# Kernel tuning notes

Measured on AMD Instinct MI355X. Metric: run time of the kernel, lower is better.

## Reference

```python
import jax, jax.numpy as jnp
import numpy as np

B, D, E, NF, FD, H = 8192, 1024, 6, 32, 32, 256
MINK, MAXK = 1, 4

def _lin(a, w, b):
    return a @ w.T + b

def setup_inputs():
    key = jax.random.key(0)
    it = iter(jax.random.split(key, 60))
    def nrm(shape, s=0.02):
        return jax.random.normal(next(it), shape, jnp.float32) * s
    z = lambda *s: jnp.zeros(s, jnp.float32)
    return dict(
        x=jax.random.normal(next(it), (B, D), jnp.float32),
        esp_patterns=nrm((E, D), 1.0),
        sim_w1=nrm((D // 2, D)), sim_b1=z(D // 2),
        sim_w2=nrm((E, D // 2)), sim_b2=z(E),
        rout_w1=nrm((D // 2, D + E)), rout_b1=z(D // 2),
        rout_w2=nrm((E, D // 2)), rout_b2=z(E),
        kpred_w1=nrm((16, 6)), kpred_b1=z(16),
        kpred_w2=nrm((1, 16)), kpred_b2=z(1),
        sp_v_w=nrm((D, D)), sp_v_b=z(D),
        sp_o_w=nrm((D, D)), sp_o_b=z(D),
        sp_q1_w=nrm((D, D)), sp_q1_b=z(D),
        sp_q2_w=nrm((D, D)), sp_q2_b=z(D),
        de_w1=nrm((H, D)), de_b1=z(H),
        de_w2=nrm((D, H)), de_b2=z(D),
        de_g_w=nrm((D, D)), de_g_b=z(D),
        cf_in_w=nrm((3 * FD, FD)), cf_in_b=z(3 * FD),
        cf_o_w=nrm((FD, FD)), cf_o_b=z(FD),
        cf_f_w=nrm((FD, FD)), cf_f_b=z(FD),
        hf_w1=nrm((H, D)), hf_b1=z(H),
        hf_w2=nrm((D, H)), hf_b2=z(D),
        tc_w=nrm((4, 1, 3), 0.2), tc_b=z(4),
        tf_w=nrm((1, 4), 0.2), tf_b=z(1),
        lt_w1=nrm((H, D)), lt_b1=z(H),
        lt_w2=nrm((D, H)), lt_b2=z(D),
        op_w=nrm((D, D)), op_b=z(D),
    )

def reference(x, esp_patterns, sim_w1, sim_b1, sim_w2, sim_b2, rout_w1, rout_b1, rout_w2, rout_b2,
              kpred_w1, kpred_b1, kpred_w2, kpred_b2, sp_v_w, sp_v_b, sp_o_w, sp_o_b,
              sp_q1_w, sp_q1_b, sp_q2_w, sp_q2_b, de_w1, de_b1, de_w2, de_b2, de_g_w, de_g_b,
              cf_in_w, cf_in_b, cf_o_w, cf_o_b, cf_f_w, cf_f_b, hf_w1, hf_b1, hf_w2, hf_b2,
              tc_w, tc_b, tf_w, tf_b, lt_w1, lt_b1, lt_w2, lt_b2, op_w, op_b):
    # ---- FeatureAnalyzer ----
    sparsity = (x == 0).astype(jnp.float32).mean(-1)
    var_u = jnp.var(x, axis=-1, ddof=1)            # torch default unbiased var
    magnitude = jnp.abs(x).max(-1)
    norm = jnp.linalg.norm(x, axis=-1)
    mean = x.mean(-1, keepdims=True)
    std = jnp.sqrt(var_u[:, None] + 1e-8)
    skew = (((x - mean) / std) ** 3).mean(-1)
    s_abs = -jnp.sort(-jnp.abs(x), axis=-1)        # descending
    top20 = int(0.2 * D)
    conc = s_abs[:, :top20].sum(-1) / (s_abs.sum(-1) + 1e-8)
    feats = jnp.stack([sparsity, var_u, magnitude, norm, skew, conc], -1)  # (B,6)
    # ---- IntelligentRouter ----
    spec = jax.nn.sigmoid(x @ esp_patterns.T + _lin(jax.nn.relu(_lin(x, sim_w1, sim_b1)), sim_w2, sim_b2))
    probs = jax.nn.softmax(_lin(jax.nn.relu(_lin(jnp.concatenate([x, spec], -1), rout_w1, rout_b1)), rout_w2, rout_b2), -1)
    k_ratio = jax.nn.sigmoid(_lin(jax.nn.relu(_lin(feats, kpred_w1, kpred_b1)), kpred_w2, kpred_b2))[:, 0]
    k_vals = MINK + (MAXK - MINK) * k_ratio
    k = jnp.clip(jnp.floor(jnp.median(k_vals)), MINK, MAXK).astype(jnp.int32)  # int(median) truncation
    tp, ti = jax.lax.top_k(probs, MAXK)
    gmask = jnp.arange(MAXK) < k
    gates = jax.nn.softmax(jnp.where(gmask, tp, -jnp.inf), -1)  # (B,MAXK)
    # ---- experts (eval mode: dropout = identity) ----
    # SparseQuadraticExpert: seq-len-1 MHA collapses to V->out projections
    att = _lin(_lin(x, sp_v_w, sp_v_b), sp_o_w, sp_o_b)
    e_sp = _lin(jax.nn.relu(_lin(att * x, sp_q1_w, sp_q1_b)), sp_q2_w, sp_q2_b)
    # DenseQuadraticExpert
    e_de = _lin(jax.nn.relu(_lin(x, de_w1, de_b1)), de_w2, de_b2) + jax.nn.sigmoid(_lin(x, de_g_w, de_g_b)) * x
    # CrossFieldQuadraticExpert: single-head attention over fields
    xf = x.reshape(-1, NF, FD)
    q, kk, v = jnp.split(_lin(xf, cf_in_w, cf_in_b), 3, axis=-1)
    attn = jax.nn.softmax(jnp.einsum('bqd,bkd->bqk', q, kk) / jnp.sqrt(jnp.float32(FD)), -1)
    att_f = _lin(jnp.einsum('bqk,bkd->bqd', attn, v), cf_o_w, cf_o_b)
    e_cf = _lin(att_f * xf, cf_f_w, cf_f_b).reshape(-1, D)
    # HighFreqQuadraticExpert
    filt = _lin(jnp.tanh(_lin(x, hf_w1, hf_b1)), hf_w2, hf_b2)
    e_hf = x + (filt - x) * x
    # TemporalQuadraticExpert (AdaptiveAvgPool1d(D) on length-D input == identity)
    conv = jax.nn.relu(jax.lax.conv_general_dilated(x[:, None, :], tc_w, (1,), [(1, 1)], dimension_numbers=('NCH', 'OIH', 'NCH')) + tc_b[None, :, None])
    wts = jax.nn.sigmoid(_lin(conv.transpose(0, 2, 1), tf_w, tf_b))[..., 0]  # (B,D)
    e_tp = (x * wts) * x
    # LongTailQuadraticExpert
    t = _lin(jax.nn.elu(_lin(x, lt_w1, lt_b1)), lt_w2, lt_b2)
    e_lt = jnp.sign(x) * jnp.sqrt(jnp.abs(t * x) + 1e-8)
    # ---- dispatch + combine ----
    stack = jnp.stack([e_sp, e_de, e_cf, e_hf, e_tp, e_lt], axis=1)  # (B,E,D)
    sel = jnp.take_along_axis(stack, ti[:, :, None], axis=1)         # (B,MAXK,D)
    comb = (gates[:, :, None] * sel).sum(1)
    return _lin(comb, op_w, op_b) + x  # output projection + residual; Identity norm (batch_norm=False)
```

## Files before the change

kernel.cpp:

```cpp
#include <hip/hip_runtime.h>
#include <stdint.h>

typedef unsigned short u16;
typedef __attribute__((ext_vector_type(2))) float f32x2;
typedef __attribute__((ext_vector_type(4))) float f32x4;
typedef __attribute__((ext_vector_type(4))) unsigned short u16x4;
typedef __attribute__((ext_vector_type(8))) short short8;

#define DEV static __device__ __forceinline__

DEV float bf2f(u16 u){ union{unsigned int i; float f;} v; v.i=((unsigned int)u)<<16; return v.f; }
DEV u16 f2bf(float f){ union{float f; unsigned int i;} v; v.f=f; unsigned int u=v.i;
  return (u16)((u + 0x7FFFu + ((u>>16)&1u))>>16); }
DEV float wred(float v){ for(int o=32;o;o>>=1) v += __shfl_xor(v,o); return v; }
DEV float wredmax(float v){ for(int o=32;o;o>>=1) v = fmaxf(v,__shfl_xor(v,o)); return v; }
DEV int wredi(int v){ for(int o=32;o;o>>=1) v += __shfl_xor(v,o); return v; }

DEV void gload16(const void* g, void* l){
  __builtin_amdgcn_global_load_lds((const __attribute__((address_space(1))) unsigned int*)g,
                                   (__attribute__((address_space(3))) unsigned int*)l, 16, 0, 0);
}

DEV float actf(int ACT, float v){
  if(ACT==1) return v>0.f?v:0.f;
  if(ACT==2) return 1.f/(1.f+__expf(-v));
  if(ACT==3) return tanhf(v);
  if(ACT==4) return v>0.f?v:(__expf(v)-1.f);
  return v;
}

__global__ void cvt_kernel(const float* __restrict__ s, u16* __restrict__ d, int n4){
  for(int i=blockIdx.x*blockDim.x+threadIdx.x; i<n4; i+=gridDim.x*blockDim.x){
    f32x4 v=((const f32x4*)s)[i];
    u16x4 o;
    #pragma unroll
    for(int j=0;j<4;++j) o[j]=f2bf(v[j]);
    ((u16x4*)d)[i]=o;
  }
}

__global__ void cvt6_kernel(
    const float* __restrict__ s0, const float* __restrict__ s1, const float* __restrict__ s2,
    const float* __restrict__ s3, const float* __restrict__ s4, const float* __restrict__ s5,
    u16* __restrict__ d0, u16* __restrict__ d1, u16* __restrict__ d2,
    u16* __restrict__ d3, u16* __restrict__ d4, u16* __restrict__ d5, int n4each){
  const float* ss[6]={s0,s1,s2,s3,s4,s5};
  u16* dd[6]={d0,d1,d2,d3,d4,d5};
  const int total=6*n4each;
  for(int i=blockIdx.x*blockDim.x+threadIdx.x; i<total; i+=gridDim.x*blockDim.x){
    int b=i/n4each, r=i-b*n4each;
    f32x4 v=((const f32x4*)ss[b])[r];
    u16x4 o;
    #pragma unroll
    for(int j=0;j<4;++j) o[j]=f2bf(v[j]);
    ((u16x4*)dd[b])[r]=o;
  }
}

__global__ void cvt_split(const float* __restrict__ s, u16* __restrict__ hi, u16* __restrict__ lo, int n4){
  for(int i=blockIdx.x*blockDim.x+threadIdx.x; i<n4; i+=gridDim.x*blockDim.x){
    f32x4 v=((const f32x4*)s)[i];
    u16x4 h,l;
    #pragma unroll
    for(int j=0;j<4;++j){ h[j]=f2bf(v[j]); l[j]=f2bf(v[j]-bf2f(h[j])); }
    ((u16x4*)hi)[i]=h; ((u16x4*)lo)[i]=l;
  }
}

__global__ void cvt_split_rw1(const float* __restrict__ src, u16* __restrict__ hi, u16* __restrict__ lo){
  for(int i=blockIdx.x*blockDim.x+threadIdx.x; i<512*1024; i+=gridDim.x*blockDim.x){
    int r=i>>10, c=i&1023;
    float v=src[(size_t)r*1030+c];
    u16 h=f2bf(v);
    hi[i]=h; lo[i]=f2bf(v-bf2f(h));
  }
}

__global__ __launch_bounds__(256) void transpose_bf(const float* __restrict__ src, u16* __restrict__ dst){
  __shared__ float t[32][33];
  const int bx=blockIdx.x&31, by=blockIdx.x>>5;
  const int lx=threadIdx.x&31, ly=threadIdx.x>>5;
  #pragma unroll
  for(int r=0;r<4;++r)
    t[ly+8*r][lx] = src[(size_t)(by*32+ly+8*r)*1024 + bx*32+lx];
  __syncthreads();
  #pragma unroll
  for(int r=0;r<4;++r)
    dst[(size_t)(bx*32+ly+8*r)*1024 + by*32+lx] = f2bf(t[lx][ly+8*r]);
}

__global__ __launch_bounds__(256) void bias_comp(const float* __restrict__ ow, const float* __restrict__ vb,
    const float* __restrict__ ob, float* __restrict__ bc){
  const int wv=threadIdx.x>>6, lane=threadIdx.x&63;
  const int rowi=blockIdx.x*4+wv;
  float s=0.f;
  const float* wr=ow+(size_t)rowi*1024;
  #pragma unroll
  for(int j=0;j<16;++j) s+=wr[j*64+lane]*vb[j*64+lane];
  s=wred(s);
  if(lane==0) bc[rowi]=ob[rowi]+s;
}

__global__ void pack_b768(const float* __restrict__ b0, const float* __restrict__ b1,
                          const float* __restrict__ b2, float* __restrict__ o){
  int i=blockIdx.x*blockDim.x+threadIdx.x;
  if(i<256) o[i]=b0[i];
  else if(i<512) o[i]=b1[i-256];
  else if(i<768) o[i]=b2[i-512];
}

__global__ void pack_b1024(const float* __restrict__ b0, const float* __restrict__ b1, float* __restrict__ o){
  int i=blockIdx.x*blockDim.x+threadIdx.x;
  if(i<512) o[i]=b0[i];
  else if(i<1024) o[i]=b1[i-512];
}

template<int ACT, int EPI>
__global__ __launch_bounds__(256) void gemm_bt(
    const u16* __restrict__ A, const u16* __restrict__ W,
    const float* __restrict__ bias, const u16* __restrict__ auxb,
    const float* __restrict__ auxf, const float* __restrict__ wsel,
    float* __restrict__ comb, void* __restrict__ Cv, int M, int N, int K, int lda)
{
  __shared__ __align__(16) u16 lA[128*64];
  __shared__ __align__(16) u16 lB[128*64];
  const int tid=threadIdx.x, lane=tid&63, wv=tid>>6;
  const int wr=wv>>1, wc=wv&1;
  const int bn=blockIdx.x*128, bm=blockIdx.y*128;
  f32x4 acc[4][4];
  #pragma unroll
  for(int m=0;m<4;++m){
    #pragma unroll
    for(int n=0;n<4;++n) acc[m][n]=(f32x4)0.f;
  }
  const int srow = wv*8 + (lane>>3);
  const int scol = (lane&7)*8;
  for(int kt=0;kt<K;kt+=64){
    #pragma unroll
    for(int i=0;i<4;++i){
      gload16(A + (size_t)(bm + i*32 + srow)*lda + kt + scol, &lA[(i*32 + wv*8)*64]);
      gload16(W + (size_t)(bn + i*32 + srow)*K + kt + scol, &lB[(i*32 + wv*8)*64]);
    }
    __syncthreads();
    #pragma unroll
    for(int kk=0;kk<2;++kk){
      const int fr=lane&15, kc=kk*32+(lane>>4)*8;
      short8 af[4], bfr[4];
      #pragma unroll
      for(int m=0;m<4;++m) af[m]=*(const short8*)&lA[(wr*64+m*16+fr)*64+kc];
      #pragma unroll
      for(int n=0;n<4;++n) bfr[n]=*(const short8*)&lB[(wc*64+n*16+fr)*64+kc];
      #pragma unroll
      for(int m=0;m<4;++m){
        #pragma unroll
        for(int n=0;n<4;++n)
          acc[m][n]=__builtin_amdgcn_mfma_f32_16x16x32_bf16(af[m],bfr[n],acc[m][n],0,0,0);
      }
    }
    __syncthreads();
  }
  const int fr=lane&15, fq=lane>>4;
  #pragma unroll
  for(int m=0;m<4;++m){
    #pragma unroll
    for(int n=0;n<4;++n){
      const int col = bn + wc*64 + n*16 + fr;
      const float bv = bias ? bias[col] : 0.f;
      #pragma unroll
      for(int j=0;j<4;++j){
        const int row = bm + wr*64 + m*16 + fq*4 + j;
        const size_t idx = (size_t)row*N+col;
        float v = acc[m][n][j] + bv;
        if(ACT==5){
          v = (col<256) ? fmaxf(v,0.f) : (col<512 ? tanhf(v) : (v>0.f?v:(__expf(v)-1.f)));
        } else v = actf(ACT, v);
        if(EPI==0){ ((u16*)Cv)[idx]=f2bf(v); }
        else if(EPI==1){ ((float*)Cv)[idx]=v; }
        else if(EPI==2){ ((u16*)Cv)[idx]=f2bf(v*auxf[idx]); }
        else if(EPI==3){ comb[idx]=wsel[row*6+0]*v; }
        else if(EPI==4){ comb[idx]+=wsel[row*6+1]*(v + bf2f(auxb[idx])*auxf[idx]); }
        else if(EPI==5){ float x0=auxf[idx]; comb[idx]+=wsel[row*6+3]*(x0+(v-x0)*x0); }
        else if(EPI==6){
          float x0=auxf[idx];
          float sg=(x0>0.f)?1.f:((x0<0.f)?-1.f:0.f);
          comb[idx]+=wsel[row*6+5]*sg*sqrtf(fabsf(v*x0)+1e-8f);
        }
        else { ((float*)Cv)[idx]=v+auxf[idx]; }
      }
    }
  }
}

__global__ __launch_bounds__(256) void gemm_split2(
    const u16* __restrict__ Ah, const u16* __restrict__ Al,
    const u16* __restrict__ Wh, const u16* __restrict__ Wl,
    const float* __restrict__ bias, float* __restrict__ C, int M, int N, int K)
{
  const int LDL=40;
  __shared__ __align__(16) u16 lAh[128*40], lAl[128*40], lBh[128*40], lBl[128*40];
  const int tid=threadIdx.x, lane=tid&63, wv=tid>>6;
  const int wr=wv>>1, wc=wv&1;
  const int nwg=gridDim.x;
  const int wg=(blockIdx.x%8)*(nwg/8)+blockIdx.x/8;
  const int bx=wg&7, by=wg>>3;
  const int bn=bx*128, bm=by*128;
  f32x4 acc[4][4];
  #pragma unroll
  for(int m=0;m<4;++m){
    #pragma unroll
    for(int n=0;n<4;++n) acc[m][n]=(f32x4)0.f;
  }
  const int srow=tid>>2, scol=(tid&3)*8;
  for(int kt=0;kt<K;kt+=32){
    short8 rah[2],ral[2],rbh[2],rbl[2];
    #pragma unroll
    for(int i=0;i<2;++i){
      size_t ao=(size_t)(bm+i*64+srow)*K+kt+scol;
      size_t bo=(size_t)(bn+i*64+srow)*K+kt+scol;
      rah[i]=*(const short8*)(Ah+ao); ral[i]=*(const short8*)(Al+ao);
      rbh[i]=*(const short8*)(Wh+bo); rbl[i]=*(const short8*)(Wl+bo);
    }
    __syncthreads();
    #pragma unroll
    for(int i=0;i<2;++i){
      int d=(i*64+srow)*LDL+scol;
      *(short8*)&lAh[d]=rah[i]; *(short8*)&lAl[d]=ral[i];
      *(short8*)&lBh[d]=rbh[i]; *(short8*)&lBl[d]=rbl[i];
    }
    __syncthreads();
    const int fr=lane&15, kc=(lane>>4)*8;
    short8 ah[4],al[4],bh[4],bl[4];
    #pragma unroll
    for(int m=0;m<4;++m){ int r=(wr*64+m*16+fr)*LDL+kc; ah[m]=*(const short8*)&lAh[r]; al[m]=*(const short8*)&lAl[r]; }
    #pragma unroll
    for(int n=0;n<4;++n){ int r=(wc*64+n*16+fr)*LDL+kc; bh[n]=*(const short8*)&lBh[r]; bl[n]=*(const short8*)&lBl[r]; }
    #pragma unroll
    for(int m=0;m<4;++m){
      #pragma unroll
      for(int n=0;n<4;++n){
        acc[m][n]=__builtin_amdgcn_mfma_f32_16x16x32_bf16(ah[m],bh[n],acc[m][n],0,0,0);
        acc[m][n]=__builtin_amdgcn_mfma_f32_16x16x32_bf16(ah[m],bl[n],acc[m][n],0,0,0);
        acc[m][n]=__builtin_amdgcn_mfma_f32_16x16x32_bf16(al[m],bh[n],acc[m][n],0,0,0);
      }
    }
  }
  const int fr=lane&15, fq=lane>>4;
  #pragma unroll
  for(int m=0;m<4;++m){
    #pragma unroll
    for(int n=0;n<4;++n){
      const int col = bn + wc*64 + n*16 + fr;
      const float bv = bias[col];
      #pragma unroll
      for(int j=0;j<4;++j){
        const int row = bm + wr*64 + m*16 + fq*4 + j;
        float v = acc[m][n][j] + bv;
        if(col<512) v=fmaxf(v,0.f);
        C[(size_t)row*N+col] = v;
      }
    }
  }
}

__global__ __launch_bounds__(256) void feats_kernel(const float* __restrict__ x,
    const float* __restrict__ kw1, const float* __restrict__ kb1,
    const float* __restrict__ kw2, const float* __restrict__ kb2,
    float* __restrict__ kvals)
{
  const int lane=threadIdx.x&63, wv=threadIdx.x>>6;
  const int row=blockIdx.x*4+wv;
  const float* xr=x+(size_t)row*1024;
  float xv[16]; unsigned int cd[16];
  float s=0.f, ss=0.f, sa=0.f, nz=0.f, amax=0.f;
  #pragma unroll
  for(int t=0;t<4;++t){
    f32x4 v=((const f32x4*)xr)[t*64+lane];
    #pragma unroll
    for(int j=0;j<4;++j){
      float f=v[j];
      union{float f;unsigned int i;} c; c.f=f;
      xv[t*4+j]=f; cd[t*4+j]=c.i&0x7fffffffu;
      s+=f; ss+=f*f; float a=fabsf(f); sa+=a; amax=fmaxf(amax,a); if(f==0.f) nz+=1.f;
    }
  }
  s=wred(s); ss=wred(ss); sa=wred(sa); nz=wred(nz); amax=wredmax(amax);
  const float mean=s/1024.f;
  const float var=(ss - s*mean)/1023.f;
  const float inv=1.f/sqrtf(var+1e-8f);
  float sk=0.f;
  #pragma unroll
  for(int j=0;j<16;++j){ float z=(xv[j]-mean)*inv; sk+=z*z*z; }
  sk=wred(sk);
  unsigned int lo=0u, hi=0x7f800000u;
  while(hi-lo>1u){
    unsigned int mid=(lo+hi)>>1;
    int c=0;
    #pragma unroll
    for(int j=0;j<16;++j) c += (cd[j] >= mid);
    c=wredi(c);
    if(c>=204) lo=mid; else hi=mid;
  }
  const unsigned int T=lo;
  float sg=0.f, cg=0.f;
  #pragma unroll
  for(int j=0;j<16;++j){ if(cd[j] > T){ sg+=fabsf(xv[j]); cg+=1.f; } }
  sg=wred(sg); cg=wred(cg);
  if(lane==0){
    union{unsigned int i;float f;} tv; tv.i=T;
    float conc=(sg + (204.f-cg)*tv.f)/(sa + 1e-8f);
    float feats[6]={ nz/1024.f, var, amax, sqrtf(ss), sk/1024.f, conc };
    float out=kb2[0];
    #pragma unroll
    for(int i=0;i<16;++i){
      float hv=kb1[i];
      #pragma unroll
      for(int j=0;j<6;++j) hv+=kw1[i*6+j]*feats[j];
      hv=fmaxf(hv,0.f);
      out+=kw2[i]*hv;
    }
    kvals[row]=1.f + 3.f*(1.f/(1.f+__expf(-out)));
  }
}

__global__ __launch_bounds__(256) void median_kernel(const float* __restrict__ kvals, int* __restrict__ kint){
  __shared__ unsigned int v[8192];
  __shared__ int hist4[4*257];
  __shared__ unsigned int selT;
  __shared__ int selR;
  const int tid=threadIdx.x, lane=tid&63, wv=tid>>6;
  for(int i=tid;i<8192;i+=256){ union{float f;unsigned int u;} c; c.f=kvals[i]; v[i]=c.u; }
  __syncthreads();
  unsigned int res[2];
  for(int t=0;t<2;++t){
    int r = 8192 - (4096+t) + 1;
    unsigned int prefix=0u;
    for(int lvl=0;lvl<4;++lvl){
      const int shift=24-lvl*8;
      const unsigned int pmask = (lvl==0)?0u:(0xFFFFFFFFu<<(shift+8));
      for(int i=tid;i<4*257;i+=256) hist4[i]=0;
      __syncthreads();
      for(int i=tid;i<8192;i+=256){
        unsigned int c=v[i];
        if((c&pmask)==prefix) atomicAdd(&hist4[wv*257+((c>>shift)&0xFFu)],1);
      }
      __syncthreads();
      if(wv==0){
        int h[4]; int ls=0;
        #pragma unroll
        for(int b=0;b<4;++b){
          int bin=lane*4+b;
          h[b]=hist4[bin]+hist4[257+bin]+hist4[514+bin]+hist4[771+bin];
          ls+=h[b];
        }
        int pfx=ls;
        #pragma unroll
        for(int off=1;off<64;off<<=1){ int tt=__shfl_up(pfx,off); if(lane>=off) pfx+=tt; }
        int total=__shfl(pfx,63);
        int cgt = total - pfx;
        #pragma unroll
        for(int b=3;b>=0;--b){
          if(cgt < r && r <= cgt + h[b]){
            selT = prefix | ((unsigned int)(lane*4+b)<<shift);
            selR = r - cgt;
          }
          cgt += h[b];
        }
      }
      __syncthreads();
      prefix=selT; r=selR;
      __syncthreads();
    }
    res[t]=prefix;
  }
  if(tid==0){
    union{unsigned int u; float f;} a,b; a.u=res[0]; b.u=res[1];
    float med=0.5f*(a.f+b.f);
    int k=(int)floorf(med);
    k = k<1?1:(k>4?4:k);
    *kint=k;
  }
}

__global__ __launch_bounds__(256) void spec_kernel(const float* __restrict__ x, const float* __restrict__ h,
    const float* __restrict__ esp, const float* __restrict__ w2, const float* __restrict__ b2,
    float* __restrict__ spec){
  const int wv=threadIdx.x>>6, lane=threadIdx.x&63;
  const int row=blockIdx.x*4+wv;
  const float* xr=x+(size_t)row*1024;
  const float* hr=h+(size_t)row*1024;
  float xv[16], hv[8];
  #pragma unroll
  for(int j=0;j<16;++j) xv[j]=xr[j*64+lane];
  #pragma unroll
  for(int j=0;j<8;++j) hv[j]=hr[j*64+lane];
  for(int e=0;e<6;++e){
    float s=0.f;
    #pragma unroll
    for(int j=0;j<16;++j) s+=xv[j]*esp[e*1024+j*64+lane];
    #pragma unroll
    for(int j=0;j<8;++j) s+=hv[j]*w2[e*512+j*64+lane];
    s=wred(s);
    if(lane==0) spec[row*6+e]=1.f/(1.f+__expf(-(s+b2[e])));
  }
}

__global__ void rout_fix(float* __restrict__ h, const float* __restrict__ spec, const float* __restrict__ rw1){
  const int total=8192*128;
  for(int i=blockIdx.x*blockDim.x+threadIdx.x;i<total;i+=gridDim.x*blockDim.x){
    int row=i>>7, j0=(i&127)*4;
    const float* sp=&spec[row*6];
    f32x4 hv=*(f32x4*)&h[(size_t)row*1024+512+j0];
    #pragma unroll
    for(int j=0;j<4;++j){
      float v=hv[j];
      int col=j0+j;
      #pragma unroll
      for(int e=0;e<6;++e) v+=sp[e]*rw1[(size_t)col*1030+1024+e];
      hv[j]=fmaxf(v,0.f);
    }
    *(f32x4*)&h[(size_t)row*1024+512+j0]=hv;
  }
}

__global__ __launch_bounds__(256) void probs_kernel(const float* __restrict__ h, const float* __restrict__ w2,
    const float* __restrict__ b2, float* __restrict__ probs){
  const int wv=threadIdx.x>>6, lane=threadIdx.x&63;
  const int row=blockIdx.x*4+wv;
  const float* hr=h+(size_t)row*1024+512;
  float hv[8];
  #pragma unroll
  for(int j=0;j<8;++j) hv[j]=hr[j*64+lane];
  float lg[6];
  #pragma unroll
  for(int e=0;e<6;++e){
    float s=0.f;
    #pragma unroll
    for(int j=0;j<8;++j) s+=hv[j]*w2[e*512+j*64+lane];
    lg[e]=wred(s)+b2[e];
  }
  if(lane==0){
    float m=lg[0];
    #pragma unroll
    for(int e=1;e<6;++e) m=fmaxf(m,lg[e]);
    float den=0.f, ex[6];
    #pragma unroll
    for(int e=0;e<6;++e){ ex[e]=__expf(lg[e]-m); den+=ex[e]; }
    #pragma unroll
    for(int e=0;e<6;++e) probs[row*6+e]=ex[e]/den;
  }
}

__global__ void gates_kernel(const float* __restrict__ probs, const int* __restrict__ kint,
                             float* __restrict__ wsel){
  const int r=blockIdx.x*blockDim.x+threadIdx.x;
  if(r>=8192) return;
  const int k=*kint;
  float p[6];
  #pragma unroll
  for(int e=0;e<6;++e) p[e]=probs[r*6+e];
  float w[6]={0,0,0,0,0,0};
  bool used[6]={false,false,false,false,false,false};
  int idx[4]; float val[4];
  #pragma unroll
  for(int j=0;j<4;++j){
    int bi=0; float bv=-1e30f;
    #pragma unroll
    for(int e=0;e<6;++e) if(!used[e] && p[e]>bv){ bv=p[e]; bi=e; }
    used[bi]=true; idx[j]=bi; val[j]=bv;
  }
  float m=val[0], den=0.f, g[4]={0,0,0,0};
  for(int j=0;j<k;++j){ g[j]=__expf(val[j]-m); den+=g[j]; }
  for(int j=0;j<k;++j) w[idx[j]]=g[j]/den;
  #pragma unroll
  for(int e=0;e<6;++e) wsel[r*6+e]=w[e];
}

__global__ __launch_bounds__(256) void cf_kernel(const float* __restrict__ x,
    const float* __restrict__ w_in, const float* __restrict__ b_in,
    const float* __restrict__ w_o, const float* __restrict__ b_o,
    const float* __restrict__ w_f, const float* __restrict__ b_f,
    const float* __restrict__ wsel, float* __restrict__ comb){
  __shared__ __align__(16) u16 smem[6400 + 4*6144];
  const int tid=threadIdx.x, wv=tid>>6, lane=tid&63;
  const int fr=lane&15, fq=lane>>4;
  for(int i=tid;i<5120;i+=256){
    float v=(i<3072)? w_in[i] : (i<4096? w_o[i-3072] : w_f[i-4096]);
    smem[(i>>5)*40 + (i&31)] = f2bf(v);
  }
  u16* wb   = smem + 6400 + wv*6144;
  float* xfl= (float*)wb;
  u16* bufA = wb + 2304;
  u16* bufB = bufA + 1280;
  u16* bufC = bufB + 1280;
  const int row = blockIdx.x*4 + wv;
  const float* xr = x + (size_t)row*1024;
  #pragma unroll
  for(int t=0;t<4;++t){
    f32x4 v = ((const f32x4*)xr)[t*64+lane];
    int e=(t*64+lane)*4;
    *(f32x4*)&xfl[(e>>5)*36 + (e&31)] = v;
  }
  __syncthreads();
  short8 xa[2];
  #pragma unroll
  for(int ft=0;ft<2;++ft){
    f32x4 a=*(const f32x4*)&xfl[(ft*16+fr)*36 + fq*8];
    f32x4 b=*(const f32x4*)&xfl[(ft*16+fr)*36 + fq*8 + 4];
    short8 s;
    s[0]=(short)f2bf(a[0]); s[1]=(short)f2bf(a[1]); s[2]=(short)f2bf(a[2]); s[3]=(short)f2bf(a[3]);
    s[4]=(short)f2bf(b[0]); s[5]=(short)f2bf(b[1]); s[6]=(short)f2bf(b[2]); s[7]=(short)f2bf(b[3]);
    xa[ft]=s;
  }
  f32x4 acc1[2][6];
  #pragma unroll
  for(int ct=0;ct<6;++ct){
    short8 wfrag=*(const short8*)&smem[(ct*16+fr)*40 + fq*8];
    #pragma unroll
    for(int ft=0;ft<2;++ft)
      acc1[ft][ct]=__builtin_amdgcn_mfma_f32_16x16x32_bf16(xa[ft],wfrag,(f32x4)0.f,0,0,0);
  }
  float bi[6];
  #pragma unroll
  for(int ct=0;ct<6;++ct) bi[ct]=b_in[ct*16+fr];
  #pragma unroll
  for(int ct=0;ct<6;++ct){
    #pragma unroll
    for(int ft=0;ft<2;++ft){
      #pragma unroll
      for(int j=0;j<4;++j){
        u16 h=f2bf(acc1[ft][ct][j]+bi[ct]);
        int rg=ft*16+fq*4+j, cg=ct*16+fr;
        if(cg<32)      bufA[rg*40+cg]=h;
        else if(cg<64) bufB[rg*40+(cg-32)]=h;
        else           bufC[(cg-64)*40+rg]=h;
      }
    }
  }
  __syncthreads();
  short8 qa0=*(const short8*)&bufA[fr*40+fq*8];
  short8 qa1=*(const short8*)&bufA[(16+fr)*40+fq*8];
  short8 kb0=*(const short8*)&bufB[fr*40+fq*8];
  short8 kb1=*(const short8*)&bufB[(16+fr)*40+fq*8];
  f32x4 aS[2][2];
  aS[0][0]=__builtin_amdgcn_mfma_f32_16x16x32_bf16(qa0,kb0,(f32x4)0.f,0,0,0);
  aS[0][1]=__builtin_amdgcn_mfma_f32_16x16x32_bf16(qa0,kb1,(f32x4)0.f,0,0,0);
  aS[1][0]=__builtin_amdgcn_mfma_f32_16x16x32_bf16(qa1,kb0,(f32x4)0.f,0,0,0);
  aS[1][1]=__builtin_amdgcn_mfma_f32_16x16x32_bf16(qa1,kb1,(f32x4)0.f,0,0,0);
  const float scale=0.17677669529663687f;
  #pragma unroll
  for(int rt=0;rt<2;++rt){
    #pragma unroll
    for(int j=0;j<4;++j){
      float e0=aS[rt][0][j]*scale, e1=aS[rt][1][j]*scale;
      float m=fmaxf(e0,e1);
      #pragma unroll
      for(int o=1;o<16;o<<=1) m=fmaxf(m,__shfl_xor(m,o));
      e0=__expf(e0-m); e1=__expf(e1-m);
      float den=e0+e1;
      #pragma unroll
      for(int o=1;o<16;o<<=1) den+=__shfl_xor(den,o);
      float inv=1.f/den;
      bufA[(rt*16+fq*4+j)*40 + fr]      = f2bf(e0*inv);
      bufA[(rt*16+fq*4+j)*40 + 16+fr]   = f2bf(e1*inv);
    }
  }
  __syncthreads();
  short8 pa0=*(const short8*)&bufA[fr*40+fq*8];
  short8 pa1=*(const short8*)&bufA[(16+fr)*40+fq*8];
  short8 vb0=*(const short8*)&bufC[fr*40+fq*8];
  short8 vb1=*(const short8*)&bufC[(16+fr)*40+fq*8];
  f32x4 aA[2][2];
  aA[0][0]=__builtin_amdgcn_mfma_f32_16x16x32_bf16(pa0,vb0,(f32x4)0.f,0,0,0);
  aA[0][1]=__builtin_amdgcn_mfma_f32_16x16x32_bf16(pa0,vb1,(f32x4)0.f,0,0,0);
  aA[1][0]=__builtin_amdgcn_mfma_f32_16x16x32_bf16(pa1,vb0,(f32x4)0.f,0,0,0);
  aA[1][1]=__builtin_amdgcn_mfma_f32_16x16x32_bf16(pa1,vb1,(f32x4)0.f,0,0,0);
  #pragma unroll
  for(int rt=0;rt<2;++rt)
    #pragma unroll
    for(int dt=0;dt<2;++dt)
      #pragma unroll
      for(int j=0;j<4;++j)
        bufB[(rt*16+fq*4+j)*40 + dt*16+fr]=f2bf(aA[rt][dt][j]);
  __syncthreads();
  short8 aa0=*(const short8*)&bufB[fr*40+fq*8];
  short8 aa1=*(const short8*)&bufB[(16+fr)*40+fq*8];
  short8 ob0=*(const short8*)&smem[(96+fr)*40+fq*8];
  short8 ob1=*(const short8*)&smem[(112+fr)*40+fq*8];
  f32x4 aF[2][2];
  aF[0][0]=__builtin_amdgcn_mfma_f32_16x16x32_bf16(aa0,ob0,(f32x4)0.f,0,0,0);
  aF[0][1]=__builtin_amdgcn_mfma_f32_16x16x32_bf16(aa0,ob1,(f32x4)0.f,0,0,0);
  aF[1][0]=__builtin_amdgcn_mfma_f32_16x16x32_bf16(aa1,ob0,(f32x4)0.f,0,0,0);
  aF[1][1]=__builtin_amdgcn_mfma_f32_16x16x32_bf16(aa1,ob1,(f32x4)0.f,0,0,0);
  float bo[2]={b_o[fr], b_o[16+fr]};
  #pragma unroll
  for(int rt=0;rt<2;++rt){
    #pragma unroll
    for(int dt=0;dt<2;++dt){
      #pragma unroll
      for(int j=0;j<4;++j){
        int fld=rt*16+fq*4+j, d=dt*16+fr;
        float attf=aF[rt][dt][j]+bo[dt];
        bufC[fld*40+d]=f2bf(attf*xfl[fld*36+d]);
      }
    }
  }
  __syncthreads();
  short8 pr0=*(const short8*)&bufC[fr*40+fq*8];
  short8 pr1=*(const short8*)&bufC[(16+fr)*40+fq*8];
  short8 fb0=*(const short8*)&smem[(128+fr)*40+fq*8];
  short8 fb1=*(const short8*)&smem[(144+fr)*40+fq*8];
  f32x4 aE[2][2];
  aE[0][0]=__builtin_amdgcn_mfma_f32_16x16x32_bf16(pr0,fb0,(f32x4)0.f,0,0,0);
  aE[0][1]=__builtin_amdgcn_mfma_f32_16x16x32_bf16(pr0,fb1,(f32x4)0.f,0,0,0);
  aE[1][0]=__builtin_amdgcn_mfma_f32_16x16x32_bf16(pr1,fb0,(f32x4)0.f,0,0,0);
  aE[1][1]=__builtin_amdgcn_mfma_f32_16x16x32_bf16(pr1,fb1,(f32x4)0.f,0,0,0);
  float bff[2]={b_f[fr], b_f[16+fr]};
  const float w2=wsel[row*6+2];
  float* cb=&comb[(size_t)row*1024];
  #pragma unroll
  for(int rt=0;rt<2;++rt){
    #pragma unroll
    for(int dt=0;dt<2;++dt){
      #pragma unroll
      for(int j=0;j<4;++j){
        int fld=rt*16+fq*4+j, d=dt*16+fr;
        cb[fld*32+d]+=w2*(aE[rt][dt][j]+bff[dt]);
      }
    }
  }
}

__global__ __launch_bounds__(256) void tp_kernel(const float* __restrict__ x,
    const float* __restrict__ wsel, const float* __restrict__ comb,
    const float* __restrict__ tcw, const float* __restrict__ tcb,
    const float* __restrict__ tfw, const float* __restrict__ tfb,
    u16* __restrict__ obf){
  __shared__ float xs[1026];
  const int row=blockIdx.x, tid=threadIdx.x;
  f32x4 u=((const f32x4*)(x+(size_t)row*1024))[tid];
  #pragma unroll
  for(int j=0;j<4;++j) xs[1+4*tid+j]=u[j];
  if(tid==0){ xs[0]=0.f; xs[1025]=0.f; }
  __syncthreads();
  const float w4=wsel[row*6+4];
  float tc[4][3], tb[4], tf[4];
  #pragma unroll
  for(int o=0;o<4;++o){
    #pragma unroll
    for(int kh=0;kh<3;++kh) tc[o][kh]=tcw[o*3+kh];
    tb[o]=tcb[o]; tf[o]=tfw[o];
  }
  const float tfb0=tfb[0];
  f32x4 cv=((const f32x4*)(comb+(size_t)row*1024))[tid];
  u16x4 ov;
  #pragma unroll
  for(int j=0;j<4;++j){
    const int d=4*tid+j;
    float pre=tfb0;
    #pragma unroll
    for(int o=0;o<4;++o){
      float c=tb[o]+tc[o][0]*xs[d]+tc[o][1]*xs[d+1]+tc[o][2]*xs[d+2];
      pre+=tf[o]*fmaxf(c,0.f);
    }
    float wt=1.f/(1.f+__expf(-pre));
    float xv=xs[1+d];
    ov[j]=f2bf(cv[j]+w4*xv*xv*wt);
  }
  ((u16x4*)(obf+(size_t)row*1024))[tid]=ov;
}

extern "C" void kernel_launch(void* const* d_in, const int* in_sizes, int n_in,
                              void* d_out, int out_size, void* d_ws, size_t ws_size,
                              hipStream_t stream)
{
  const float* x     =(const float*)d_in[0];
  const float* esp   =(const float*)d_in[1];
  const float* sim_w1=(const float*)d_in[2],  *sim_b1=(const float*)d_in[3];
  const float* sim_w2=(const float*)d_in[4],  *sim_b2=(const float*)d_in[5];
  const float* rout_w1=(const float*)d_in[6], *rout_b1=(const float*)d_in[7];
  const float* rout_w2=(const float*)d_in[8], *rout_b2=(const float*)d_in[9];
  const float* kw1=(const float*)d_in[10], *kb1=(const float*)d_in[11];
  const float* kw2=(const float*)d_in[12], *kb2=(const float*)d_in[13];
  const float* spv_w=(const float*)d_in[14], *spv_b=(const float*)d_in[15];
  const float* spo_w=(const float*)d_in[16], *spo_b=(const float*)d_in[17];
  const float* spq1_w=(const float*)d_in[18], *spq1_b=(const float*)d_in[19];
  const float* spq2_w=(const float*)d_in[20], *spq2_b=(const float*)d_in[21];
  const float* de_w1=(const float*)d_in[22], *de_b1=(const float*)d_in[23];
  const float* de_w2=(const float*)d_in[24], *de_b2=(const float*)d_in[25];
  const float* de_gw=(const float*)d_in[26], *de_gb=(const float*)d_in[27];
  const float* cf_inw=(const float*)d_in[28], *cf_inb=(const float*)d_in[29];
  const float* cf_ow=(const float*)d_in[30], *cf_ob=(const float*)d_in[31];
  const float* cf_fw=(const float*)d_in[32], *cf_fb=(const float*)d_in[33];
  const float* hf_w1=(const float*)d_in[34], *hf_b1=(const float*)d_in[35];
  const float* hf_w2=(const float*)d_in[36], *hf_b2=(const float*)d_in[37];
  const float* tc_w=(const float*)d_in[38], *tc_b=(const float*)d_in[39];
  const float* tf_w=(const float*)d_in[40], *tf_b=(const float*)d_in[41];
  const float* lt_w1=(const float*)d_in[42], *lt_b1=(const float*)d_in[43];
  const float* lt_w2=(const float*)d_in[44], *lt_b2=(const float*)d_in[45];
  const float* op_w=(const float*)d_in[46], *op_b=(const float*)d_in[47];
  float* out=(float*)d_out;
  (void)in_sizes; (void)n_in; (void)out_size; (void)ws_size;

  constexpr int NB=8192;
  const size_t BD=(size_t)NB*1024;
  char* base=(char*)d_ws; size_t off=0;
  auto carve=[&](size_t n)->void*{ void* q=base+off; off+=(n+255)&~(size_t)255; return q; };
  float* comb =(float*)carve(BD*4);
  u16*  bufA =(u16*)carve(BD*2);
  u16*  bufB =(u16*)carve(BD*2);
  u16*  x_hi =(u16*)carve(BD*2);
  u16*  x_lo =(u16*)carve(BD*2);
  float* h1024=(float*)carve(BD*4);
  u16*  h768 =(u16*)carve((size_t)NB*768*2);
  u16* w1024h=(u16*)carve((size_t)1024*1024*2);
  u16* w1024l=(u16*)carve((size_t)1024*1024*2);
  u16* spv_bf =(u16*)carve((size_t)1024*1024*2);
  u16* spo_bf =(u16*)carve((size_t)1024*1024*2);
  u16* spq1_bf=(u16*)carve((size_t)1024*1024*2);
  u16* spq2_bf=(u16*)carve((size_t)1024*1024*2);
  u16* w768_bf=(u16*)carve((size_t)768*1024*2);
  u16* dew2_bf=(u16*)carve((size_t)1024*256*2);
  u16* degw_bf=(u16*)carve((size_t)1024*1024*2);
  u16* hfw2_bf=(u16*)carve((size_t)1024*256*2);
  u16* ltw2_bf=(u16*)carve((size_t)1024*256*2);
  u16* opw_bf =(u16*)carve((size_t)1024*1024*2);
  u16* spvT_bf=(u16*)carve((size_t)1024*1024*2);
  float* bc   =(float*)carve((size_t)1024*4);
  float* b768 =(float*)carve((size_t)768*4);
  float* b1024=(float*)carve((size_t)1024*4);
  float* spec=(float*)carve((size_t)NB*6*4);
  float* probs=(float*)carve((size_t)NB*6*4);
  float* wsel=(float*)carve((size_t)NB*6*4);
  float* kvals=(float*)carve((size_t)NB*4);
  int*   kint=(int*)carve(256);

  const dim3 blk(256);
  const dim3 gEW(2048);
  auto cgrid=[&](int n4)->dim3{ int g=(n4+255)/256; return dim3(g>2048?2048:g); };

  cvt_split<<<cgrid(2097152),blk,0,stream>>>(x, x_hi, x_lo, 2097152);
  cvt_split<<<cgrid(131072),blk,0,stream>>>(sim_w1, w1024h, w1024l, 131072);
  cvt_split_rw1<<<cgrid(131072),blk,0,stream>>>(rout_w1, w1024h+524288, w1024l+524288);
  cvt6_kernel<<<cgrid(6*262144),blk,0,stream>>>(spv_w,spo_w,spq1_w,spq2_w,de_gw,op_w,
                                                spv_bf,spo_bf,spq1_bf,spq2_bf,degw_bf,opw_bf, 262144);
  cvt6_kernel<<<cgrid(6*65536),blk,0,stream>>>(de_w1,de_w2,hf_w1,hf_w2,lt_w1,lt_w2,
                                               w768_bf,dew2_bf,w768_bf+262144,hfw2_bf,w768_bf+524288,ltw2_bf, 65536);
  transpose_bf<<<dim3(1024),blk,0,stream>>>(spv_w, spvT_bf);
  bias_comp<<<dim3(256),blk,0,stream>>>(spo_w, spv_b, spo_b, bc);
  pack_b768<<<dim3(3),blk,0,stream>>>(de_b1, hf_b1, lt_b1, b768);
  pack_b1024<<<dim3(4),blk,0,stream>>>(sim_b1, rout_b1, b1024);

  feats_kernel<<<dim3(2048),blk,0,stream>>>(x, kw1,kb1,kw2,kb2, kvals);
  median_kernel<<<dim3(1),blk,0,stream>>>(kvals, kint);
  gemm_split2<<<dim3(512),blk,0,stream>>>(x_hi,x_lo, w1024h,w1024l, b1024, h1024, NB,1024,1024);
  spec_kernel<<<gEW,blk,0,stream>>>(x, h1024, esp, sim_w2, sim_b2, spec);
  rout_fix<<<gEW,blk,0,stream>>>(h1024, spec, rout_w1);
  probs_kernel<<<gEW,blk,0,stream>>>(h1024, rout_w2, rout_b2, probs);
  gates_kernel<<<dim3(32),blk,0,stream>>>(probs, kint, wsel);

  gemm_bt<0,1><<<dim3(8,8),blk,0,stream>>>(spo_bf, spvT_bf, nullptr, nullptr, nullptr, nullptr, nullptr, h1024, 1024,1024,1024,1024);
  cvt_kernel<<<cgrid(262144),blk,0,stream>>>(h1024, spv_bf, 262144);

  gemm_bt<0,2><<<dim3(8,64),blk,0,stream>>>(x_hi, spv_bf, bc, nullptr, x, nullptr, nullptr, bufB, NB,1024,1024,1024);
  gemm_bt<1,0><<<dim3(8,64),blk,0,stream>>>(bufB, spq1_bf, spq1_b, nullptr, nullptr, nullptr, nullptr, bufA, NB,1024,1024,1024);
  gemm_bt<0,3><<<dim3(8,64),blk,0,stream>>>(bufA, spq2_bf, spq2_b, nullptr, nullptr, wsel, comb, nullptr, NB,1024,1024,1024);

  gemm_bt<5,0><<<dim3(6,64),blk,0,stream>>>(x_hi, w768_bf, b768, nullptr, nullptr, nullptr, nullptr, h768, NB,768,1024,1024);

  gemm_bt<2,0><<<dim3(8,64),blk,0,stream>>>(x_hi, degw_bf, de_gb, nullptr, nullptr, nullptr, nullptr, bufB, NB,1024,1024,1024);
  gemm_bt<0,4><<<dim3(8,64),blk,0,stream>>>(h768, dew2_bf, de_b2, bufB, x, wsel, comb, nullptr, NB,1024,256,768);

  cf_kernel<<<dim3(2048),blk,0,stream>>>(x, cf_inw, cf_inb, cf_ow, cf_ob, cf_fw, cf_fb, wsel, comb);

  gemm_bt<0,5><<<dim3(8,64),blk,0,stream>>>(h768+256, hfw2_bf, hf_b2, nullptr, x, wsel, comb, nullptr, NB,1024,256,768);

  gemm_bt<0,6><<<dim3(8,64),blk,0,stream>>>(h768+512, ltw2_bf, lt_b2, nullptr, x, wsel, comb, nullptr, NB,1024,256,768);

  tp_kernel<<<dim3(NB),blk,0,stream>>>(x, wsel, comb, tc_w, tc_b, tf_w, tf_b, bufB);

  gemm_bt<0,7><<<dim3(8,64),blk,0,stream>>>(bufB, opw_bf, op_b, nullptr, x, nullptr, nullptr, out, NB,1024,1024,1024);
}
```

Measured before the change: 604.8 us.

## Store combine accumulator in bf16, read bf16 x in epilogues, swizzle GEMM tiles

The shared combine accumulator becomes bf16 instead of fp32, which halves its read-modify-write traffic across the expert GEMM epilogues and the cf and tp kernels. The EPI 2, 5 and 6 epilogues now read x from its bf16 copy instead of fp32. gemm_bt also remaps block indices in groups of 8 to change which tiles run together, aimed at better L2 reuse. The cost is repeated bf16 rounding of the accumulated combine sum, which adds numerical error.

New measurement: 580.0 us. 4.1% less time.

```diff
diff --git a/kernel.cpp b/kernel.cpp
--- a/kernel.cpp
+++ b/kernel.cpp
@@ -120,13 +120,18 @@
     const u16* __restrict__ A, const u16* __restrict__ W,
     const float* __restrict__ bias, const u16* __restrict__ auxb,
     const float* __restrict__ auxf, const float* __restrict__ wsel,
-    float* __restrict__ comb, void* __restrict__ Cv, int M, int N, int K, int lda)
+    u16* __restrict__ comb, void* __restrict__ Cv, int M, int N, int K, int lda)
 {
   __shared__ __align__(16) u16 lA[128*64];
   __shared__ __align__(16) u16 lB[128*64];
   const int tid=threadIdx.x, lane=tid&63, wv=tid>>6;
   const int wr=wv>>1, wc=wv&1;
-  const int bn=blockIdx.x*128, bm=blockIdx.y*128;
+  const int gx=gridDim.x;
+  const int nwg=gx*gridDim.y;
+  const int flat=blockIdx.y*gx+blockIdx.x;
+  const int chunk=nwg>>3;
+  const int nf=(flat&7)*chunk + (flat>>3);
+  const int bn=(nf%gx)*128, bm=(nf/gx)*128;
   f32x4 acc[4][4];
   #pragma unroll
   for(int m=0;m<4;++m){
@@ -176,14 +181,14 @@
         } else v = actf(ACT, v);
         if(EPI==0){ ((u16*)Cv)[idx]=f2bf(v); }
         else if(EPI==1){ ((float*)Cv)[idx]=v; }
-        else if(EPI==2){ ((u16*)Cv)[idx]=f2bf(v*auxf[idx]); }
-        else if(EPI==3){ comb[idx]=wsel[row*6+0]*v; }
-        else if(EPI==4){ comb[idx]+=wsel[row*6+1]*(v + bf2f(auxb[idx])*auxf[idx]); }
-        else if(EPI==5){ float x0=auxf[idx]; comb[idx]+=wsel[row*6+3]*(x0+(v-x0)*x0); }
+        else if(EPI==2){ ((u16*)Cv)[idx]=f2bf(v*bf2f(auxb[idx])); }
+        else if(EPI==3){ comb[idx]=f2bf(wsel[row*6+0]*v); }
+        else if(EPI==4){ comb[idx]=f2bf(bf2f(comb[idx])+wsel[row*6+1]*(v + bf2f(auxb[idx])*auxf[idx])); }
+        else if(EPI==5){ float x0=bf2f(auxb[idx]); comb[idx]=f2bf(bf2f(comb[idx])+wsel[row*6+3]*(x0+(v-x0)*x0)); }
         else if(EPI==6){
-          float x0=auxf[idx];
+          float x0=bf2f(auxb[idx]);
           float sg=(x0>0.f)?1.f:((x0<0.f)?-1.f:0.f);
-          comb[idx]+=wsel[row*6+5]*sg*sqrtf(fabsf(v*x0)+1e-8f);
+          comb[idx]=f2bf(bf2f(comb[idx])+wsel[row*6+5]*sg*sqrtf(fabsf(v*x0)+1e-8f));
         }
         else { ((float*)Cv)[idx]=v+auxf[idx]; }
       }
@@ -479,7 +484,7 @@
     const float* __restrict__ w_in, const float* __restrict__ b_in,
     const float* __restrict__ w_o, const float* __restrict__ b_o,
     const float* __restrict__ w_f, const float* __restrict__ b_f,
-    const float* __restrict__ wsel, float* __restrict__ comb){
+    const float* __restrict__ wsel, u16* __restrict__ comb){
   __shared__ __align__(16) u16 smem[6400 + 4*6144];
   const int tid=threadIdx.x, wv=tid>>6, lane=tid&63;
   const int fr=lane&15, fq=lane>>4;
@@ -616,7 +621,7 @@
   aE[1][1]=__builtin_amdgcn_mfma_f32_16x16x32_bf16(pr1,fb1,(f32x4)0.f,0,0,0);
   float bff[2]={b_f[fr], b_f[16+fr]};
   const float w2=wsel[row*6+2];
-  float* cb=&comb[(size_t)row*1024];
+  u16* cb=&comb[(size_t)row*1024];
   #pragma unroll
   for(int rt=0;rt<2;++rt){
     #pragma unroll
@@ -624,14 +629,15 @@
       #pragma unroll
       for(int j=0;j<4;++j){
         int fld=rt*16+fq*4+j, d=dt*16+fr;
-        cb[fld*32+d]+=w2*(aE[rt][dt][j]+bff[dt]);
+        u16 old=cb[fld*32+d];
+        cb[fld*32+d]=f2bf(bf2f(old)+w2*(aE[rt][dt][j]+bff[dt]));
       }
     }
   }
 }
 
 __global__ __launch_bounds__(256) void tp_kernel(const float* __restrict__ x,
-    const float* __restrict__ wsel, const float* __restrict__ comb,
+    const float* __restrict__ wsel, const u16* __restrict__ comb,
     const float* __restrict__ tcw, const float* __restrict__ tcb,
     const float* __restrict__ tfw, const float* __restrict__ tfb,
     u16* __restrict__ obf){
@@ -651,7 +657,7 @@
     tb[o]=tcb[o]; tf[o]=tfw[o];
   }
   const float tfb0=tfb[0];
-  f32x4 cv=((const f32x4*)(comb+(size_t)row*1024))[tid];
+  u16x4 cv=((const u16x4*)(comb+(size_t)row*1024))[tid];
   u16x4 ov;
   #pragma unroll
   for(int j=0;j<4;++j){
@@ -664,7 +670,7 @@
     }
     float wt=1.f/(1.f+__expf(-pre));
     float xv=xs[1+d];
-    ov[j]=f2bf(cv[j]+w4*xv*xv*wt);
+    ov[j]=f2bf(bf2f(cv[j])+w4*xv*xv*wt);
   }
   ((u16x4*)(obf+(size_t)row*1024))[tid]=ov;
 }
@@ -705,7 +711,7 @@
   const size_t BD=(size_t)NB*1024;
   char* base=(char*)d_ws; size_t off=0;
   auto carve=[&](size_t n)->void*{ void* q=base+off; off+=(n+255)&~(size_t)255; return q; };
-  float* comb =(float*)carve(BD*4);
+  u16*  comb =(u16*)carve(BD*2);
   u16*  bufA =(u16*)carve(BD*2);
   u16*  bufB =(u16*)carve(BD*2);
   u16*  x_hi =(u16*)carve(BD*2);
@@ -761,7 +767,7 @@
   gemm_bt<0,1><<<dim3(8,8),blk,0,stream>>>(spo_bf, spvT_bf, nullptr, nullptr, nullptr, nullptr, nullptr, h1024, 1024,1024,1024,1024);
   cvt_kernel<<<cgrid(262144),blk,0,stream>>>(h1024, spv_bf, 262144);
 
-  gemm_bt<0,2><<<dim3(8,64),blk,0,stream>>>(x_hi, spv_bf, bc, nullptr, x, nullptr, nullptr, bufB, NB,1024,1024,1024);
+  gemm_bt<0,2><<<dim3(8,64),blk,0,stream>>>(x_hi, spv_bf, bc, x_hi, nullptr, nullptr, nullptr, bufB, NB,1024,1024,1024);
   gemm_bt<1,0><<<dim3(8,64),blk,0,stream>>>(bufB, spq1_bf, spq1_b, nullptr, nullptr, nullptr, nullptr, bufA, NB,1024,1024,1024);
   gemm_bt<0,3><<<dim3(8,64),blk,0,stream>>>(bufA, spq2_bf, spq2_b, nullptr, nullptr, wsel, comb, nullptr, NB,1024,1024,1024);
 
@@ -772,9 +778,9 @@
 
   cf_kernel<<<dim3(2048),blk,0,stream>>>(x, cf_inw, cf_inb, cf_ow, cf_ob, cf_fw, cf_fb, wsel, comb);
 
-  gemm_bt<0,5><<<dim3(8,64),blk,0,stream>>>(h768+256, hfw2_bf, hf_b2, nullptr, x, wsel, comb, nullptr, NB,1024,256,768);
-
-  gemm_bt<0,6><<<dim3(8,64),blk,0,stream>>>(h768+512, ltw2_bf, lt_b2, nullptr, x, wsel, comb, nullptr, NB,1024,256,768);
+  gemm_bt<0,5><<<dim3(8,64),blk,0,stream>>>(h768+256, hfw2_bf, hf_b2, x_hi, nullptr, wsel, comb, nullptr, NB,1024,256,768);
+
+  gemm_bt<0,6><<<dim3(8,64),blk,0,stream>>>(h768+512, ltw2_bf, lt_b2, x_hi, nullptr, wsel, comb, nullptr, NB,1024,256,768);
 
   tp_kernel<<<dim3(NB),blk,0,stream>>>(x, wsel, comb, tc_w, tc_b, tf_w, tf_b, bufB);
 
```
